# Kernel tuning notes

Measured on AMD Instinct MI355X. Metric: run time of the kernel, lower is better.

Reference implementation:

```python
import jax, jax.numpy as jnp
import numpy as np

E = 1152        # hidden_size
I = 4304        # intermediate_size
H = 16          # num_attention_heads
HD = E // H     # head_dim = 72
EPS = 1e-6
NEG = float(np.finfo(np.float32).min)


def setup_inputs() -> dict:
    key = jax.random.key(0)
    ks = jax.random.split(key, 12)
    B, S = 32, 4096
    sc = 0.02
    return {
        "hidden_state": jax.random.normal(ks[0], (B, S, E), jnp.float32),
        "attention_mask": jnp.ones((B, S), jnp.int32),
        "probe": jax.random.normal(ks[1], (1, 1, E), jnp.float32),
        "in_proj_w": jax.random.normal(ks[2], (3 * E, E), jnp.float32) * sc,
        "in_proj_b": jax.random.normal(ks[3], (3 * E,), jnp.float32) * sc,
        "out_w": jax.random.normal(ks[4], (E, E), jnp.float32) * sc,
        "out_b": jax.random.normal(ks[5], (E,), jnp.float32) * sc,
        "ln_g": jnp.ones((E,), jnp.float32),
        "ln_b": jnp.zeros((E,), jnp.float32),
        "fc1_w": jax.random.normal(ks[6], (I, E), jnp.float32) * sc,
        "fc1_b": jax.random.normal(ks[7], (I,), jnp.float32) * sc,
        "fc2_w": jax.random.normal(ks[8], (E, I), jnp.float32) * sc,
        "fc2_b": jax.random.normal(ks[9], (E,), jnp.float32) * sc,
    }


def _forward(hidden_state, attention_mask, probe, in_proj_w, in_proj_b,
             out_w, out_b, ln_g, ln_b, fc1_w, fc1_b, fc2_w, fc2_b):
    B, S, _ = hidden_state.shape
    wq, wk, wv = jnp.split(in_proj_w, 3, axis=0)   # each [E, E]
    bq, bk, bv = jnp.split(in_proj_b, 3, axis=0)

    # probe query: identical across batch -> compute once. [H, HD]
    q = (probe[0, 0] @ wq.T + bq).reshape(H, HD)
    k = (hidden_state @ wk.T + bk).reshape(B, S, H, HD)
    v = (hidden_state @ wv.T + bv).reshape(B, S, H, HD)

    # additive mask: (1 - mask) * finfo.min, broadcast over heads. [B, S]
    addmask = (1.0 - attention_mask.astype(hidden_state.dtype)) * NEG

    scale = 1.0 / jnp.sqrt(jnp.asarray(HD, hidden_state.dtype))
    scores = jnp.einsum("hd,bshd->bhs", q, k) * scale + addmask[:, None, :]
    attn = jax.nn.softmax(scores, axis=-1)                 # [B, H, S]
    pooled = jnp.einsum("bhs,bshd->bhd", attn, v).reshape(B, E)
    pooled = pooled @ out_w.T + out_b                      # [B, E]

    residual = pooled
    mu = jnp.mean(pooled, axis=-1, keepdims=True)
    var = jnp.mean(jnp.square(pooled - mu), axis=-1, keepdims=True)
    x = (pooled - mu) * jax.lax.rsqrt(var + EPS) * ln_g + ln_b

    h = jax.nn.gelu(x @ fc1_w.T + fc1_b, approximate=True)  # gelu_pytorch_tanh
    mlp_out = h @ fc2_w.T + fc2_b
    return residual + mlp_out                               # [B, E]


def reference(hidden_state, attention_mask, probe, in_proj_w, in_proj_b,
              out_w, out_b, ln_g, ln_b, fc1_w, fc1_b, fc2_w, fc2_b):
    return _forward(hidden_state, attention_mask, probe, in_proj_w, in_proj_b,
                    out_w, out_b, ln_g, ln_b, fc1_w, fc1_b, fc2_w, fc2_b)
```

## Files before the change

kernel.cpp:

```cpp
#include <hip/hip_runtime.h>
#include <math.h>

#define E 1152
#define H 16
#define HD 72
#define B 32
#define S 4096
#define IDIM 4304
#define NSL 16

#define NEGF (-3.402823466e38f)
#define SCALE 0.1178511301977579f

typedef short short8 __attribute__((ext_vector_type(8)));
typedef float f32x4 __attribute__((ext_vector_type(4)));
typedef unsigned int uint4v __attribute__((ext_vector_type(4)));

#define GLOAD_LDS16(gp, lp) __builtin_amdgcn_global_load_lds( \
    (const __attribute__((address_space(1))) unsigned int*)(gp), \
    (__attribute__((address_space(3))) unsigned int*)(lp), 16, 0, 0)

#define LGKM_BAR() do { asm volatile("s_waitcnt lgkmcnt(0)" ::: "memory"); \
                        __builtin_amdgcn_s_barrier(); } while(0)

__device__ __forceinline__ unsigned int cvtpk_bf16(float lo, float hi){
  unsigned int r;
  asm("v_cvt_pk_bf16_f32 %0, %1, %2" : "=v"(r) : "v"(lo), "v"(hi));
  return r;
}

__device__ __forceinline__ unsigned short f2bf(float x){
  unsigned int u = __float_as_uint(x);
  u = (u + 0x7fffu + ((u >> 16) & 1u)) >> 16;
  return (unsigned short)u;
}

__device__ __forceinline__ float wredsum(float v){
  v += __shfl_xor(v,32); v += __shfl_xor(v,16); v += __shfl_xor(v,8);
  v += __shfl_xor(v,4);  v += __shfl_xor(v,2);  v += __shfl_xor(v,1);
  return v;
}

__global__ void k_q(const float* __restrict__ probe, const float* __restrict__ ipw,
                    const float* __restrict__ ipb, float* __restrict__ q){
  int tid = threadIdx.x, lane = tid & 63, w = tid >> 6;
  int j = blockIdx.x*4 + w;
  const float2* wr = (const float2*)(ipw + (size_t)j*E);
  const float2* pr = (const float2*)probe;
  float s = 0.f;
  #pragma unroll
  for (int t=0;t<9;++t){
    int e2 = lane + 64*t;
    float2 a = pr[e2], b = wr[e2];
    s = fmaf(a.x, b.x, fmaf(a.y, b.y, s));
  }
  s = wredsum(s);
  if (lane==0) q[j] = s + ipb[j];
}

__global__ void k_qk(const float* __restrict__ q, const float* __restrict__ ipw,
                     const float* __restrict__ ipb, unsigned short* __restrict__ qkfrag,
                     float* __restrict__ cb){
  int idx = blockIdx.x*256 + threadIdx.x;
  int h = idx / E, e = idx % E;
  float s = 0.f;
  #pragma unroll 8
  for (int d=0; d<HD; ++d)
    s = fmaf(q[h*HD+d], ipw[(size_t)(E + h*HD + d)*E + e], s);
  int kk = e >> 5, g = (e >> 3) & 3, j = e & 7;
  qkfrag[(size_t)kk*512 + (g*16 + h)*8 + j] = f2bf(s);
  if (idx < H){
    float c = 0.f;
    for (int d=0; d<HD; ++d) c = fmaf(q[idx*HD+d], ipb[E + idx*HD + d], c);
    cb[idx] = c;
  }
}

__global__ __launch_bounds__(256) void k_fused(
    const float* __restrict__ hidden, const unsigned short* __restrict__ qkfrag,
    const float* __restrict__ cb, const int* __restrict__ mask,
    float* __restrict__ part, float* __restrict__ part_ml){
  __shared__ float smemf[38480];
  float* D1       = smemf + 36864;
  float* f_lds    = smemf + 37952;
  float* wgt_lds  = smemf + 37968;
  float* mask_lds = smemf + 38224;

  int tid = threadIdx.x, lane = tid & 63, w = tid >> 6;
  int b = blockIdx.x >> 4, sl = blockIdx.x & 15;
  int s0 = sl * 256;

  mask_lds[tid] = (1.0f - (float)mask[(size_t)b*S + s0 + tid]) * NEGF;

  short8 qkf[9];
  {
    const short8* qf = (const short8*)qkfrag;
    #pragma unroll
    for (int kk=0;kk<9;++kk) qkf[kk] = qf[(9*w + kk)*64 + lane];
  }

  int soff[18];
  #pragma unroll
  for (int i=0;i<18;++i){
    int d = (w*18 + i)*256 + lane*4;
    int r = d / 1152;
    int o = d - r*1152;
    int fb = o >> 2;
    soff[i] = r*1152 + ((fb ^ (r & 7)) << 2);
  }

  float2 acc[4][9];
  #pragma unroll
  for (int j=0;j<4;++j)
    #pragma unroll
    for (int k=0;k<9;++k){ acc[j][k].x = 0.f; acc[j][k].y = 0.f; }

  float m = -INFINITY, lsum = 0.f;
  float scb = SCALE * cb[lane & 15];
  const float* hbase = hidden + ((size_t)b*S + s0)*E;

  int rA = lane & 15, gA = lane >> 4, rxA = rA & 7;
  int fbA0 = 72*w + 2*gA;
  int lb4 = lane >> 2, le = 2*(lane & 3);
  int fbP0 = 2*lb4 + (le >> 2), lo2 = le & 3;

  {
    const float* src = hbase;
    #pragma unroll
    for (int i=0;i<18;++i)
      GLOAD_LDS16(src + soff[i], smemf + (w*18 + i)*256);
  }

  for (int st=0; st<16; ++st){
    __syncthreads();
    float* tp = smemf + (st & 1)*18432;
    if (st+1 < 16){
      const float* src = hbase + (size_t)(st+1)*18432;
      float* dst = smemf + ((st+1) & 1)*18432;
      #pragma unroll
      for (int i=0;i<18;++i)
        GLOAD_LDS16(src + soff[i], dst + (w*18 + i)*256);
    }

    f32x4 d1 = {0.f,0.f,0.f,0.f};
    #pragma unroll
    for (int kk=0;kk<9;++kk){
      int fb0 = fbA0 + 8*kk;
      const float4 fa = *(const float4*)(tp + rA*1152 + ((fb0     ^ rxA) << 2));
      const float4 fc = *(const float4*)(tp + rA*1152 + (((fb0+1) ^ rxA) << 2));
      uint4v u;
      u[0] = cvtpk_bf16(fa.x, fa.y);
      u[1] = cvtpk_bf16(fa.z, fa.w);
      u[2] = cvtpk_bf16(fc.x, fc.y);
      u[3] = cvtpk_bf16(fc.z, fc.w);
      d1 = __builtin_amdgcn_mfma_f32_16x16x32_bf16(
             __builtin_bit_cast(short8, u), qkf[kk], d1, 0, 0, 0);
    }
    #pragma unroll
    for (int q=0;q<4;++q)
      D1[(w*16 + gA*4 + q)*17 + rA] = d1[q];

    LGKM_BAR();

    if (w == 0){
      int hh = lane & 15, gg = lane >> 4;
      float v[4];
      #pragma unroll
      for (int q=0;q<4;++q){
        int R = gg*4 + q;
        float raw = D1[R*17+hh] + D1[(16+R)*17+hh]
                  + D1[(32+R)*17+hh] + D1[(48+R)*17+hh];
        v[q] = fmaf(raw, SCALE, scb) + mask_lds[st*16 + R];
      }
      float sm = fmaxf(fmaxf(v[0],v[1]), fmaxf(v[2],v[3]));
      sm = fmaxf(sm, __shfl_xor(sm,16));
      sm = fmaxf(sm, __shfl_xor(sm,32));
      float f = 1.0f;
      if (__any(sm > m + 8.0f)){
        float mn = fmaxf(m, sm);
        f = __expf(m - mn);
        m = mn; lsum *= f;
      }
      if (lane < 16) f_lds[lane] = f;
      #pragma unroll
      for (int q=0;q<4;++q){
        float wq = __expf(v[q] - m);
        lsum += wq;
        wgt_lds[(gg*4+q)*16 + hh] = wq;
      }
    }

    LGKM_BAR();

    {
      const float4 fv = *(const float4*)(f_lds + 4*w);
      if (fv.x!=1.f || fv.y!=1.f || fv.z!=1.f || fv.w!=1.f){
        #pragma unroll
        for (int k=0;k<9;++k){
          acc[0][k].x*=fv.x; acc[0][k].y*=fv.x;
          acc[1][k].x*=fv.y; acc[1][k].y*=fv.y;
          acc[2][k].x*=fv.z; acc[2][k].y*=fv.z;
          acc[3][k].x*=fv.w; acc[3][k].y*=fv.w;
        }
      }
      #pragma unroll
      for (int r2=0; r2<16; ++r2){
        const float4 wg = *(const float4*)(wgt_lds + r2*16 + 4*w);
        int rx2 = r2 & 7;
        int rowb = r2*1152;
        #pragma unroll
        for (int k=0;k<9;++k){
          const float2 hv = *(const float2*)(tp + rowb + (((fbP0 + 32*k) ^ rx2) << 2) + lo2);
          acc[0][k].x = fmaf(wg.x, hv.x, acc[0][k].x); acc[0][k].y = fmaf(wg.x, hv.y, acc[0][k].y);
          acc[1][k].x = fmaf(wg.y, hv.x, acc[1][k].x); acc[1][k].y = fmaf(wg.y, hv.y, acc[1][k].y);
          acc[2][k].x = fmaf(wg.z, hv.x, acc[2][k].x); acc[2][k].y = fmaf(wg.z, hv.y, acc[2][k].y);
          acc[3][k].x = fmaf(wg.w, hv.x, acc[3][k].x); acc[3][k].y = fmaf(wg.w, hv.y, acc[3][k].y);
        }
      }
    }
  }

  if (w == 0){
    float lt = lsum + __shfl_xor(lsum, 16);
    lt += __shfl_xor(lt, 32);
    if (lane < 16){
      size_t o = ((size_t)(b*NSL + sl)*16 + lane)*2;
      part_ml[o] = m; part_ml[o+1] = lt;
    }
  }
  #pragma unroll
  for (int j=0;j<4;++j){
    float2* dst = (float2*)(part + ((size_t)(b*NSL + sl)*H + 4*w + j)*E);
    #pragma unroll
    for (int k=0;k<9;++k) dst[lane + 64*k] = acc[j][k];
  }
}

__global__ void k_ctxred(const float* __restrict__ part, const float* __restrict__ part_ml,
                         float* __restrict__ ctx){
  int idx = blockIdx.x*256 + threadIdx.x;
  int b = idx / (H*E); int he = idx % (H*E); int h = he / E;
  float M = -INFINITY, L = 0.f;
  #pragma unroll 4
  for (int c = 0; c < NSL; ++c){
    size_t o = ((size_t)(b*NSL + c)*16 + h)*2;
    float om = part_ml[o], ol = part_ml[o+1];
    float nm = fmaxf(M, om);
    L = L*__expf(M - nm) + ol*__expf(om - nm);
    M = nm;
  }
  float invL = 1.0f / L;
  float s = 0.f;
  #pragma unroll 4
  for (int sl=0; sl<NSL; ++sl){
    float scl = __expf(part_ml[((size_t)(b*NSL + sl)*16 + h)*2] - M) * invL;
    s = fmaf(part[(size_t)(b*NSL+sl)*H*E + he], scl, s);
  }
  ctx[idx] = s;
}

__global__ __launch_bounds__(256) void k_pool(
    const float* __restrict__ ctx, const float* __restrict__ ipw,
    const float* __restrict__ ipb, float* __restrict__ pooled){
  __shared__ float red[4][32];
  int tid = threadIdx.x, lane = tid & 63, w = tid >> 6;
  int j = blockIdx.x;
  int h = j / HD;
  const float2* wr = (const float2*)(ipw + (size_t)2*E*E + (size_t)j*E);
  float acc[32];
  #pragma unroll
  for (int b_=0;b_<32;++b_) acc[b_]=0.f;
  for (int t=w; t<9; t+=4){
    int e2 = lane + 64*t;
    float2 wv = wr[e2];
    #pragma unroll
    for (int b_=0;b_<32;++b_){
      float2 cv = *(const float2*)(ctx + (size_t)(b_*H + h)*E + 2*e2);
      acc[b_] = fmaf(wv.x, cv.x, fmaf(wv.y, cv.y, acc[b_]));
    }
  }
  #pragma unroll
  for (int b_=0;b_<32;++b_){
    float s = wredsum(acc[b_]);
    if (lane==b_) red[w][b_] = s;
  }
  __syncthreads();
  if (tid < 32){
    float s = red[0][tid] + red[1][tid] + red[2][tid] + red[3][tid];
    pooled[(size_t)tid*E + j] = s + ipb[2*E + j];
  }
}

__global__ __launch_bounds__(256) void k_outproj(
    const float* __restrict__ pooled, const float* __restrict__ ow,
    const float* __restrict__ ob, float* __restrict__ resid){
  __shared__ float red[4][32];
  int tid = threadIdx.x, lane = tid & 63, w = tid >> 6;
  int i = blockIdx.x;
  const float2* wr = (const float2*)(ow + (size_t)i*E);
  float acc[32];
  #pragma unroll
  for (int b_=0;b_<32;++b_) acc[b_]=0.f;
  for (int t=w; t<9; t+=4){
    int e2 = lane + 64*t;
    float2 wv = wr[e2];
    #pragma unroll
    for (int b_=0;b_<32;++b_){
      float2 pv = *(const float2*)(pooled + (size_t)b_*E + 2*e2);
      acc[b_] = fmaf(wv.x, pv.x, fmaf(wv.y, pv.y, acc[b_]));
    }
  }
  #pragma unroll
  for (int b_=0;b_<32;++b_){
    float s = wredsum(acc[b_]);
    if (lane==b_) red[w][b_] = s;
  }
  __syncthreads();
  if (tid < 32){
    float s = red[0][tid] + red[1][tid] + red[2][tid] + red[3][tid];
    resid[(size_t)tid*E + i] = s + ob[i];
  }
}

__global__ void k_ln(const float* __restrict__ resid, const float* __restrict__ g,
                     const float* __restrict__ be, float* __restrict__ x){
  __shared__ float red[8];
  int b = blockIdx.x, tid = threadIdx.x, lane = tid & 63, w = tid >> 6;
  const float* r = resid + (size_t)b*E;
  float s = 0.f, s2 = 0.f;
  for (int e=tid; e<E; e+=256){ float v = r[e]; s += v; s2 = fmaf(v,v,s2); }
  s = wredsum(s); s2 = wredsum(s2);
  if (lane==0){ red[w]=s; red[4+w]=s2; }
  __syncthreads();
  float S1 = red[0]+red[1]+red[2]+red[3];
  float S2 = red[4]+red[5]+red[6]+red[7];
  float mu  = S1*(1.0f/E);
  float var = S2*(1.0f/E) - mu*mu;
  float inv = rsqrtf(var + 1e-6f);
  for (int e=tid; e<E; e+=256){
    float v = (r[e]-mu)*inv;
    x[(size_t)b*E + e] = v*g[e] + be[e];
  }
}

__device__ __forceinline__ float gelu_tanh(float u){
  float u3 = u*u*u;
  float t = tanhf(0.7978845608028654f*(u + 0.044715f*u3));
  return 0.5f*u*(1.0f+t);
}

__global__ __launch_bounds__(256) void k_fc1(
    const float* __restrict__ x, const float* __restrict__ w1,
    const float* __restrict__ b1, float* __restrict__ h1){
  __shared__ float red[4][2][32];
  int tid = threadIdx.x, lane = tid & 63, w = tid >> 6;
  int i0 = blockIdx.x*2;
  float acc[2][32];
  #pragma unroll
  for (int ii=0;ii<2;++ii)
    #pragma unroll
    for (int b_=0;b_<32;++b_) acc[ii][b_]=0.f;
  const float2* w1a = (const float2*)(w1 + (size_t)i0*E);
  const float2* w1b = (const float2*)(w1 + (size_t)(i0+1)*E);
  for (int t=w; t<9; t+=4){
    int e2 = lane + 64*t;
    float2 f0 = w1a[e2];
    float2 f1 = w1b[e2];
    #pragma unroll
    for (int b_=0;b_<32;++b_){
      float2 xv = *(const float2*)(x + (size_t)b_*E + 2*e2);
      acc[0][b_] = fmaf(f0.x, xv.x, fmaf(f0.y, xv.y, acc[0][b_]));
      acc[1][b_] = fmaf(f1.x, xv.x, fmaf(f1.y, xv.y, acc[1][b_]));
    }
  }
  #pragma unroll
  for (int ii=0;ii<2;++ii)
    #pragma unroll
    for (int b_=0;b_<32;++b_){
      float s = wredsum(acc[ii][b_]);
      if (lane==b_) red[w][ii][b_] = s;
    }
  __syncthreads();
  if (tid < 64){
    int b_ = tid & 31, ii = tid >> 5;
    float s = red[0][ii][b_] + red[1][ii][b_] + red[2][ii][b_] + red[3][ii][b_];
    h1[(size_t)b_*IDIM + i0 + ii] = gelu_tanh(s + b1[i0+ii]);
  }
}

__global__ __launch_bounds__(256) void k_fc2(
    const float* __restrict__ h1, const float* __restrict__ w2,
    const float* __restrict__ b2, const float* __restrict__ resid,
    float* __restrict__ out){
  __shared__ float red[4][2][32];
  int tid = threadIdx.x, lane = tid & 63, w = tid >> 6;
  int i0 = blockIdx.x*2;
  float acc[2][32];
  #pragma unroll
  for (int ii=0;ii<2;++ii)
    #pragma unroll
    for (int b_=0;b_<32;++b_) acc[ii][b_]=0.f;
  for (int t=w; t<68; t+=4){
    int e = lane + 64*t;
    if (e < IDIM){
      float f0 = w2[(size_t)i0*IDIM + e];
      float f1 = w2[(size_t)(i0+1)*IDIM + e];
      #pragma unroll
      for (int b_=0;b_<32;++b_){
        float hvv = h1[(size_t)b_*IDIM + e];
        acc[0][b_] = fmaf(f0, hvv, acc[0][b_]);
        acc[1][b_] = fmaf(f1, hvv, acc[1][b_]);
      }
    }
  }
  #pragma unroll
  for (int ii=0;ii<2;++ii)
    #pragma unroll
    for (int b_=0;b_<32;++b_){
      float s = wredsum(acc[ii][b_]);
      if (lane==b_) red[w][ii][b_] = s;
    }
  __syncthreads();
  if (tid < 64){
    int b_ = tid & 31, ii = tid >> 5;
    float s = red[0][ii][b_] + red[1][ii][b_] + red[2][ii][b_] + red[3][ii][b_];
    int i = i0 + ii;
    out[(size_t)b_*E + i] = resid[(size_t)b_*E + i] + s + b2[i];
  }
}

extern "C" void kernel_launch(void* const* d_in, const int* in_sizes, int n_in,
                              void* d_out, int out_size, void* d_ws, size_t ws_size,
                              hipStream_t stream){
  const float* hidden = (const float*)d_in[0];
  const int*   mask   = (const int*)d_in[1];
  const float* probe  = (const float*)d_in[2];
  const float* ipw    = (const float*)d_in[3];
  const float* ipb    = (const float*)d_in[4];
  const float* ow     = (const float*)d_in[5];
  const float* ob     = (const float*)d_in[6];
  const float* ln_g   = (const float*)d_in[7];
  const float* ln_b   = (const float*)d_in[8];
  const float* w1     = (const float*)d_in[9];
  const float* b1     = (const float*)d_in[10];
  const float* w2     = (const float*)d_in[11];
  const float* b2     = (const float*)d_in[12];
  float* out = (float*)d_out;
  float* ws  = (float*)d_ws;

  size_t off = 0;
  float* q  = ws + off; off += E;
  float* cb = ws + off; off += 16;
  unsigned short* qkfrag = (unsigned short*)(ws + off); off += 9216;
  float* part_ml = ws + off; off += 32*NSL*16*2;
  float* part    = ws + off; off += (size_t)B*NSL*H*E;
  float* ctx     = ws + off; off += (size_t)B*H*E;
  float* pooled  = ws + off; off += (size_t)B*E;
  float* resid   = ws + off; off += (size_t)B*E;
  float* x       = ws + off; off += (size_t)B*E;
  float* h1      = ws + off;

  k_q       <<<288, 256, 0, stream>>>(probe, ipw, ipb, q);
  k_qk      <<<72, 256, 0, stream>>>(q, ipw, ipb, qkfrag, cb);
  k_fused   <<<B*NSL, 256, 0, stream>>>(hidden, qkfrag, cb, mask, part, part_ml);
  k_ctxred  <<<2304, 256, 0, stream>>>(part, part_ml, ctx);
  k_pool    <<<1152, 256, 0, stream>>>(ctx, ipw, ipb, pooled);
  k_outproj <<<1152, 256, 0, stream>>>(pooled, ow, ob, resid);
  k_ln      <<<32, 256, 0, stream>>>(resid, ln_g, ln_b, x);
  k_fc1     <<<2152, 256, 0, stream>>>(x, w1, b1, h1);
  k_fc2     <<<576, 256, 0, stream>>>(h1, w2, b2, resid, out);
}
```

Baseline: 368.0 us.

## Stage hidden tile as bf16 in LDS and use MFMA for weighted V accumulation

The fused attention kernel now loads hidden-state tiles through registers, converts them to bf16 once, and stores them in LDS in an MFMA-friendly blocked layout. This replaces the async global-to-LDS fp32 copies and the per-use conversion. The softmax weights are packed to bf16, and the weighted sum over the hidden tile runs on 16x16x32 bf16 MFMA instead of scalar FMAs. Global loads for the next tile are split across the stage to overlap with compute. The cost is bf16 rounding of the weights and values in the pooled sum, plus more register pressure from the staging buffers.

```diff
diff --git a/kernel.cpp b/kernel.cpp
--- a/kernel.cpp
+++ b/kernel.cpp
@@ -15,10 +15,6 @@
 typedef short short8 __attribute__((ext_vector_type(8)));
 typedef float f32x4 __attribute__((ext_vector_type(4)));
 typedef unsigned int uint4v __attribute__((ext_vector_type(4)));
-
-#define GLOAD_LDS16(gp, lp) __builtin_amdgcn_global_load_lds( \
-    (const __attribute__((address_space(1))) unsigned int*)(gp), \
-    (__attribute__((address_space(3))) unsigned int*)(lp), 16, 0, 0)
 
 #define LGKM_BAR() do { asm volatile("s_waitcnt lgkmcnt(0)" ::: "memory"); \
                         __builtin_amdgcn_s_barrier(); } while(0)
@@ -80,11 +76,11 @@
     const float* __restrict__ hidden, const unsigned short* __restrict__ qkfrag,
     const float* __restrict__ cb, const int* __restrict__ mask,
     float* __restrict__ part, float* __restrict__ part_ml){
-  __shared__ float smemf[38480];
-  float* D1       = smemf + 36864;
-  float* f_lds    = smemf + 37952;
-  float* wgt_lds  = smemf + 37968;
-  float* mask_lds = smemf + 38224;
+  __shared__ __attribute__((aligned(16))) char smem[79680];
+  float*    D1      = (float*)(smem + 73728);
+  float*    f_lds   = (float*)(smem + 78080);
+  unsigned* wgtA    = (unsigned*)(smem + 78144);
+  float*    mask_lds= (float*)(smem + 78656);
 
   int tid = threadIdx.x, lane = tid & 63, w = tid >> 6;
   int b = blockIdx.x >> 4, sl = blockIdx.x & 15;
@@ -99,62 +95,62 @@
     for (int kk=0;kk<9;++kk) qkf[kk] = qf[(9*w + kk)*64 + lane];
   }
 
-  int soff[18];
+  int dstb[18];
   #pragma unroll
   for (int i=0;i<18;++i){
-    int d = (w*18 + i)*256 + lane*4;
-    int r = d / 1152;
-    int o = d - r*1152;
-    int fb = o >> 2;
-    soff[i] = r*1152 + ((fb ^ (r & 7)) << 2);
-  }
-
-  float2 acc[4][9];
-  #pragma unroll
-  for (int j=0;j<4;++j)
-    #pragma unroll
-    for (int k=0;k<9;++k){ acc[j][k].x = 0.f; acc[j][k].y = 0.f; }
+    int f = tid + 256*i;
+    int r = f / 288, c4 = f - r*288;
+    dstb[i] = ((r>>2)*72 + (c4>>2))*128 + (r&3)*32 + (c4&3)*8;
+  }
+
+  int rA = lane & 15, gA = lane >> 4;
+  int aoff = ((rA>>2)*72 + 18*w + (gA>>1))*128 + (rA&3)*32 + (gA&1)*16;
+  int g2 = gA & 1;
+  int pvb0 = ((2*g2    )*72 + 18*w)*128 + ((lane&15)>>1)*4;
+  int pvb1 = ((2*g2 + 1)*72 + 18*w)*128 + ((lane&15)>>1)*4;
+  unsigned sel = 0x05040100u + (unsigned)(lane&1)*0x02020202u;
+  int h15 = lane & 15;
+
+  f32x4 acc[18];
+  #pragma unroll
+  for (int c=0;c<18;++c) acc[c] = (f32x4){0.f,0.f,0.f,0.f};
 
   float m = -INFINITY, lsum = 0.f;
-  float scb = SCALE * cb[lane & 15];
+  float scb = SCALE * cb[h15];
   const float* hbase = hidden + ((size_t)b*S + s0)*E;
 
-  int rA = lane & 15, gA = lane >> 4, rxA = rA & 7;
-  int fbA0 = 72*w + 2*gA;
-  int lb4 = lane >> 2, le = 2*(lane & 3);
-  int fbP0 = 2*lb4 + (le >> 2), lo2 = le & 3;
-
   {
-    const float* src = hbase;
-    #pragma unroll
-    for (int i=0;i<18;++i)
-      GLOAD_LDS16(src + soff[i], smemf + (w*18 + i)*256);
+    const float4* srcp = (const float4*)hbase;
+    float4 stg[18];
+    #pragma unroll
+    for (int i=0;i<18;++i) stg[i] = srcp[tid + 256*i];
+    #pragma unroll
+    for (int i=0;i<18;++i){
+      unsigned u0 = cvtpk_bf16(stg[i].x, stg[i].y);
+      unsigned u1 = cvtpk_bf16(stg[i].z, stg[i].w);
+      *(uint2*)(smem + dstb[i]) = make_uint2(u0, u1);
+    }
   }
 
   for (int st=0; st<16; ++st){
     __syncthreads();
-    float* tp = smemf + (st & 1)*18432;
+    char* tp = (st & 1) ? (smem + 36864) : smem;
+    char* tn = (st & 1) ? smem : (smem + 36864);
+    const float4* srcp = (const float4*)(hbase + (size_t)(st+1)*18432);
+
+    float4 stg0[9];
     if (st+1 < 16){
-      const float* src = hbase + (size_t)(st+1)*18432;
-      float* dst = smemf + ((st+1) & 1)*18432;
-      #pragma unroll
-      for (int i=0;i<18;++i)
-        GLOAD_LDS16(src + soff[i], dst + (w*18 + i)*256);
-    }
+      #pragma unroll
+      for (int i=0;i<9;++i) stg0[i] = srcp[tid + 256*i];
+    }
+    __builtin_amdgcn_sched_barrier(0);
 
     f32x4 d1 = {0.f,0.f,0.f,0.f};
     #pragma unroll
     for (int kk=0;kk<9;++kk){
-      int fb0 = fbA0 + 8*kk;
-      const float4 fa = *(const float4*)(tp + rA*1152 + ((fb0     ^ rxA) << 2));
-      const float4 fc = *(const float4*)(tp + rA*1152 + (((fb0+1) ^ rxA) << 2));
-      uint4v u;
-      u[0] = cvtpk_bf16(fa.x, fa.y);
-      u[1] = cvtpk_bf16(fa.z, fa.w);
-      u[2] = cvtpk_bf16(fc.x, fc.y);
-      u[3] = cvtpk_bf16(fc.z, fc.w);
+      uint4v ub = *(const uint4v*)(tp + aoff + 256*kk);
       d1 = __builtin_amdgcn_mfma_f32_16x16x32_bf16(
-             __builtin_bit_cast(short8, u), qkf[kk], d1, 0, 0, 0);
+             __builtin_bit_cast(short8, ub), qkf[kk], d1, 0, 0, 0);
     }
     #pragma unroll
     for (int q=0;q<4;++q)
@@ -182,40 +178,70 @@
         m = mn; lsum *= f;
       }
       if (lane < 16) f_lds[lane] = f;
-      #pragma unroll
-      for (int q=0;q<4;++q){
-        float wq = __expf(v[q] - m);
-        lsum += wq;
-        wgt_lds[(gg*4+q)*16 + hh] = wq;
-      }
+      float w0 = __expf(v[0] - m), w1 = __expf(v[1] - m);
+      float w2 = __expf(v[2] - m), w3 = __expf(v[3] - m);
+      lsum += w0 + w1 + w2 + w3;
+      wgtA[(gg*16 + hh)*2    ] = cvtpk_bf16(w0, w1);
+      wgtA[(gg*16 + hh)*2 + 1] = cvtpk_bf16(w2, w3);
     }
 
     LGKM_BAR();
 
+    float4 stg1[9];
+    if (st+1 < 16){
+      #pragma unroll
+      for (int i=0;i<9;++i) stg1[i] = srcp[tid + 256*i + 2304];
+    }
+    __builtin_amdgcn_sched_barrier(0);
+
     {
-      const float4 fv = *(const float4*)(f_lds + 4*w);
+      uint4v ua;
+      if (gA < 2){
+        ua[0] = wgtA[((2*gA  )*16 + h15)*2    ];
+        ua[1] = wgtA[((2*gA  )*16 + h15)*2 + 1];
+        ua[2] = wgtA[((2*gA+1)*16 + h15)*2    ];
+        ua[3] = wgtA[((2*gA+1)*16 + h15)*2 + 1];
+      } else {
+        ua[0]=0u; ua[1]=0u; ua[2]=0u; ua[3]=0u;
+      }
+      short8 afrag = __builtin_bit_cast(short8, ua);
+
+      const float4 fv = *(const float4*)(f_lds + gA*4);
       if (fv.x!=1.f || fv.y!=1.f || fv.z!=1.f || fv.w!=1.f){
         #pragma unroll
-        for (int k=0;k<9;++k){
-          acc[0][k].x*=fv.x; acc[0][k].y*=fv.x;
-          acc[1][k].x*=fv.y; acc[1][k].y*=fv.y;
-          acc[2][k].x*=fv.z; acc[2][k].y*=fv.z;
-          acc[3][k].x*=fv.w; acc[3][k].y*=fv.w;
+        for (int c=0;c<18;++c){
+          acc[c][0]*=fv.x; acc[c][1]*=fv.y; acc[c][2]*=fv.z; acc[c][3]*=fv.w;
         }
       }
       #pragma unroll
-      for (int r2=0; r2<16; ++r2){
-        const float4 wg = *(const float4*)(wgt_lds + r2*16 + 4*w);
-        int rx2 = r2 & 7;
-        int rowb = r2*1152;
-        #pragma unroll
-        for (int k=0;k<9;++k){
-          const float2 hv = *(const float2*)(tp + rowb + (((fbP0 + 32*k) ^ rx2) << 2) + lo2);
-          acc[0][k].x = fmaf(wg.x, hv.x, acc[0][k].x); acc[0][k].y = fmaf(wg.x, hv.y, acc[0][k].y);
-          acc[1][k].x = fmaf(wg.y, hv.x, acc[1][k].x); acc[1][k].y = fmaf(wg.y, hv.y, acc[1][k].y);
-          acc[2][k].x = fmaf(wg.z, hv.x, acc[2][k].x); acc[2][k].y = fmaf(wg.z, hv.y, acc[2][k].y);
-          acc[3][k].x = fmaf(wg.w, hv.x, acc[3][k].x); acc[3][k].y = fmaf(wg.w, hv.y, acc[3][k].y);
-        }
+      for (int c=0;c<18;++c){
+        const unsigned* p0 = (const unsigned*)(tp + pvb0 + 128*c);
+        const unsigned* p1 = (const unsigned*)(tp + pvb1 + 128*c);
+        unsigned a0 = p0[0], a1 = p0[8], a2 = p0[16], a3 = p0[24];
+        unsigned b0 = p1[0], b1 = p1[8], b2 = p1[16], b3 = p1[24];
+        uint4v ub;
+        ub[0] = __builtin_amdgcn_perm(a1, a0, sel);
+        ub[1] = __builtin_amdgcn_perm(a3, a2, sel);
+        ub[2] = __builtin_amdgcn_perm(b1, b0, sel);
+        ub[3] = __builtin_amdgcn_perm(b3, b2, sel);
+        acc[c] = __builtin_amdgcn_mfma_f32_16x16x32_bf16(
+                   afrag, __builtin_bit_cast(short8, ub), acc[c], 0, 0, 0);
+      }
+    }
+    __builtin_amdgcn_sched_barrier(0);
+
+    if (st+1 < 16){
+      #pragma unroll
+      for (int i=0;i<9;++i){
+        unsigned u0 = cvtpk_bf16(stg0[i].x, stg0[i].y);
+        unsigned u1 = cvtpk_bf16(stg0[i].z, stg0[i].w);
+        *(uint2*)(tn + dstb[i]) = make_uint2(u0, u1);
+      }
+      #pragma unroll
+      for (int i=0;i<9;++i){
+        unsigned u0 = cvtpk_bf16(stg1[i].x, stg1[i].y);
+        unsigned u1 = cvtpk_bf16(stg1[i].z, stg1[i].w);
+        *(uint2*)(tn + dstb[9+i]) = make_uint2(u0, u1);
       }
     }
   }
@@ -228,11 +254,15 @@
       part_ml[o] = m; part_ml[o+1] = lt;
     }
   }
-  #pragma unroll
-  for (int j=0;j<4;++j){
-    float2* dst = (float2*)(part + ((size_t)(b*NSL + sl)*H + 4*w + j)*E);
-    #pragma unroll
-    for (int k=0;k<9;++k) dst[lane + 64*k] = acc[j][k];
+  {
+    float* pp = part + ((size_t)(b*NSL + sl))*H*E;
+    #pragma unroll
+    for (int c=0;c<18;++c){
+      int e = 16*(18*w + c) + h15;
+      #pragma unroll
+      for (int q=0;q<4;++q)
+        pp[(size_t)(gA*4 + q)*E + e] = acc[c][q];
+    }
   }
 }
 
```

Result: faster. 309.8 us (-15.8%).
